# Kernel optimization log

Hardware: AMD Instinct MI355X
Metric: run time of the kernel (lower is better)

Reference implementation:

```python
import jax, jax.numpy as jnp
import numpy as np

B = 4096
MAXN = 25  # maxnfpoc, also MaxPool1d kernel size


def _w(k, fan_in, fan_out):
    return jax.random.normal(k, (fan_in, fan_out), jnp.float32) * (1.0 / np.sqrt(fan_in))


def setup_inputs() -> dict:
    key = jax.random.key(0)
    ks = jax.random.split(key, 8)
    fpoc = jax.random.normal(ks[0], (B, MAXN, 2), jnp.float32)
    nfpc = jax.random.randint(ks[1], (B,), 3, MAXN + 1, jnp.int32)
    return {
        "fpoc": fpoc,
        "cw1": _w(ks[2], 2, 64),    "cb1": jnp.zeros((64,), jnp.float32),
        "cw2": _w(ks[3], 64, 128),  "cb2": jnp.zeros((128,), jnp.float32),
        "lw1": _w(ks[4], 256, 512), "lb1": jnp.zeros((512,), jnp.float32),
        "lw2": _w(ks[5], 512, 1024),"lb2": jnp.zeros((1024,), jnp.float32),
        "fw":  _w(ks[6], 1024, 511),"fb":  jnp.zeros((511,), jnp.float32),
        "nfpc": nfpc,
    }


def reference(fpoc, cw1, cb1, cw2, cb2, lw1, lb1, lw2, lb2, fw, fb, nfpc):
    act = jax.nn.relu
    # corner MLP: act on all but last layer
    h = act(fpoc @ cw1 + cb1)
    h = h @ cw2 + cb2                               # [B, MAXN, 128]
    # vectorized ragged line pairing: (pt_i, pt_{(i+1) % nfpc}), zeros beyond nfpc
    idx = jnp.arange(MAXN)
    valid = idx[None, :] < nfpc[:, None]            # [B, MAXN]
    nxt = (idx[None, :] + 1) % nfpc[:, None]        # [B, MAXN]
    h_next = jnp.take_along_axis(h, nxt[:, :, None], axis=1)
    pair = jnp.where(valid[:, :, None], jnp.concatenate([h, h_next], axis=-1), 0.0)  # [B, MAXN, 256]
    # line MLP
    l = act(pair @ lw1 + lb1)
    l = l @ lw2 + lb2                               # [B, MAXN, 1024]
    # pad invalid slots with line 0's feature, then maxpool over all MAXN slots
    lp = jnp.where(valid[:, :, None], l, l[:, 0:1, :])
    pooled = jnp.max(lp, axis=1)                    # [B, 1024]
    # fp MLP: single linear (loop body empty for len==1), then unsqueeze
    out = pooled @ fw + fb                          # [B, 511]
    return out[:, None, :]                          # [B, 1, 511]
```

## Files before the change

### kernel.cpp

```cpp
#include <hip/hip_runtime.h>

typedef __attribute__((ext_vector_type(8))) short bf16x8;
typedef __attribute__((ext_vector_type(4))) float f32x4;
typedef __attribute__((ext_vector_type(8))) unsigned short u16x8;

#define MFMA16(a, b, c) __builtin_amdgcn_mfma_f32_16x16x32_bf16((a), (b), (c), 0, 0, 0)

static __device__ __forceinline__ unsigned short f2bf(float x) {
    union { float f; unsigned u; } v; v.f = x;
    unsigned r = v.u + 0x7fffu + ((v.u >> 16) & 1u);
    return (unsigned short)(r >> 16);
}

static __device__ __forceinline__ void gload16(const void* g, void* l) {
    __builtin_amdgcn_global_load_lds(
        (const __attribute__((address_space(1))) unsigned int*)g,
        (__attribute__((address_space(3))) unsigned int*)l, 16, 0, 0);
}

static __device__ __forceinline__ bool tile_assign(int bid, int apm, int npc_log2,
                                                   int& pr, int& pc) {
    const int k = bid & 7, j = bid >> 3;
    const int T = apm << npc_log2;
    const int lo = (T * k) >> 3, hi = (T * (k + 1)) >> 3;
    const int tix = lo + j;
    if (tix >= hi) return false;
    pc = tix & ((1 << npc_log2) - 1);
    pr = tix >> npc_log2;
    return true;
}

#define WS_POOLED   0u
#define WS_LW1T     8388608u
#define WS_LW2T     8650752u
#define WS_FWT      9699328u
#define WS_SCAN     10747904u
#define WS_HEADER   10764544u
#define WS_RMB      10764800u
#define WS_RMNEXT   11174400u
#define WS_HC       11584000u
#define WS_SCRATCH  37798400u
#define WS_HID      71352832u

__global__ void convert_scan_kernel(
    const float* __restrict__ lw1, const float* __restrict__ lw2, const float* __restrict__ fw,
    short* __restrict__ lw1t, short* __restrict__ lw2t, short* __restrict__ fwt,
    const int* __restrict__ nfpc, int* __restrict__ scanv, int* __restrict__ header)
{
    const int bid = blockIdx.x;
    const int t = threadIdx.x;
    if (bid == 288) {
        __shared__ int s[256];
        int loc[16]; int sum = 0;
        #pragma unroll
        for (int i = 0; i < 16; ++i) { loc[i] = sum; sum += nfpc[t * 16 + i]; }
        s[t] = sum;
        __syncthreads();
        for (int d = 1; d < 256; d <<= 1) {
            int v = (t >= d) ? s[t - d] : 0;
            __syncthreads();
            s[t] += v;
            __syncthreads();
        }
        int excl = (t == 0) ? 0 : s[t - 1];
        #pragma unroll
        for (int i = 0; i < 16; ++i) scanv[t * 16 + i] = excl + loc[i];
        if (t == 255) {
            int M = s[255];
            scanv[4096] = M;
            header[0] = M;
            header[1] = (M + 127) & ~127;
        }
        return;
    }

    const float* src; short* dst;
    int srcN, nmax, dstK, n0, k0;
    if (bid < 32) {
        int tn = bid >> 2, tk = bid & 3;
        src = lw1; srcN = 512; nmax = 512; dst = lw1t; dstK = 256;
        n0 = tn * 64; k0 = tk * 64;
    } else if (bid < 160) {
        int u = bid - 32; int tn = u >> 3, tk = u & 7;
        src = lw2; srcN = 1024; nmax = 1024; dst = lw2t; dstK = 512;
        n0 = tn * 64; k0 = tk * 64;
    } else {
        int u = bid - 160; int tn = u >> 4, tk = u & 15;
        src = fw; srcN = 511; nmax = 511; dst = fwt; dstK = 1024;
        n0 = tn * 64; k0 = tk * 64;
    }

    __shared__ float lds[64 * 65];
    for (int e = t; e < 4096; e += 256) {
        int r = e >> 6, c = e & 63;
        int n = n0 + c;
        lds[r * 65 + c] = (n < nmax) ? src[(size_t)(k0 + r) * srcN + n] : 0.0f;
    }
    __syncthreads();
    for (int e = t; e < 1024; e += 256) {
        int rn = e >> 4, c4 = (e & 15) * 4;
        ushort4 o;
        o.x = f2bf(lds[(c4 + 0) * 65 + rn]);
        o.y = f2bf(lds[(c4 + 1) * 65 + rn]);
        o.z = f2bf(lds[(c4 + 2) * 65 + rn]);
        o.w = f2bf(lds[(c4 + 3) * 65 + rn]);
        *(ushort4*)&dst[(size_t)(n0 + rn) * dstK + k0 + c4] = o;
    }
}

__global__ void rowmap_kernel(const int* __restrict__ scanv, const int* __restrict__ header,
                              int* __restrict__ rm_b, int* __restrict__ rm_next,
                              unsigned short* __restrict__ h_c)
{
    int r = blockIdx.x * 256 + threadIdx.x;
    if (r >= 102400) return;
    const int Mc = header[0];
    if (r >= Mc) {
        rm_b[r] = -1; rm_next[r] = r;
        if (r < header[1]) {
            ushort4 z = {0, 0, 0, 0};
            #pragma unroll
            for (int j = 0; j < 128; j += 4)
                *(ushort4*)&h_c[(size_t)r * 128 + j] = z;
        }
        return;
    }
    int lo = 0, hi = 4096;
    while (hi - lo > 1) { int mid = (lo + hi) >> 1; if (scanv[mid] <= r) lo = mid; else hi = mid; }
    int b = lo, ii = r - scanv[b], n = scanv[b + 1] - scanv[b];
    rm_b[r] = b;
    rm_next[r] = (ii + 1 == n) ? scanv[b] : r + 1;
}

#define CB 4
__global__ __launch_bounds__(256, 2) void corner_kernel(
    const float* __restrict__ fpoc,
    const float* __restrict__ cw1, const float* __restrict__ cb1,
    const float* __restrict__ cw2, const float* __restrict__ cb2,
    const int* __restrict__ scanv,
    unsigned short* __restrict__ h_c)
{
    __shared__ float s_h1[CB * 25 * 64];
    __shared__ float s_cw2[64 * 128];
    __shared__ float s_x[CB * 25 * 2];
    __shared__ int s_off[CB], s_nn[CB];
    const int b0 = blockIdx.x * CB;
    const int t = threadIdx.x;

    for (int e = t; e < 64 * 128; e += 256) s_cw2[e] = cw2[e];
    for (int e = t; e < CB * 50; e += 256) s_x[e] = fpoc[b0 * 50 + e];
    if (t < CB) { int o = scanv[b0 + t]; s_off[t] = o; s_nn[t] = scanv[b0 + t + 1] - o; }
    __syncthreads();

    for (int e = t; e < CB * 25 * 64; e += 256) {
        int i = e >> 6, j = e & 63;
        float v = s_x[i * 2] * cw1[j] + s_x[i * 2 + 1] * cw1[64 + j] + cb1[j];
        s_h1[e] = fmaxf(v, 0.f);
    }
    __syncthreads();

    for (int e = t; e < CB * 25 * 32; e += 256) {
        int i = e >> 5, j4 = (e & 31) * 4;
        int g = i / 25, ii = i % 25;
        if (ii < s_nn[g]) {
            float4 a = *(const float4*)(cb2 + j4);
            const float* h1r = &s_h1[i * 64];
            #pragma unroll
            for (int k = 0; k < 64; ++k) {
                float hv = h1r[k];
                float4 wv = *(const float4*)(s_cw2 + k * 128 + j4);
                a.x += hv * wv.x; a.y += hv * wv.y; a.z += hv * wv.z; a.w += hv * wv.w;
            }
            ushort4 o;
            o.x = f2bf(a.x); o.y = f2bf(a.y); o.z = f2bf(a.z); o.w = f2bf(a.w);
            *(ushort4*)&h_c[(size_t)(s_off[g] + ii) * 128 + j4] = o;
        }
    }
}

__global__ __launch_bounds__(256, 4) void gemm1_kernel(
    const unsigned short* __restrict__ h_c,
    const short* __restrict__ lw1t,
    const float* __restrict__ lb1,
    const int* __restrict__ rm_next,
    const int* __restrict__ header,
    unsigned short* __restrict__ hid,
    int row0, int pm)
{
    __shared__ __align__(16) char smem[33280];
    __shared__ int s_next[128];

    const int Mcp = header[1];
    int rem = Mcp - row0;
    int apm = (rem <= 0) ? 0 : min(pm, (rem + 127) >> 7);
    int pr, pc;
    if (!tile_assign(blockIdx.x, apm, 2, pr, pc)) return;
    const int Rl = pr * 128;
    const int R = row0 + Rl;

    const int t = threadIdx.x;
    const int w = t >> 6, l = t & 63, q = l >> 4, ln = l & 15;
    const int wr = w >> 1, wc = w & 1;
    char* ldsA = smem;
    char* ldsB = smem + 16384;

    if (t < 128) s_next[t] = rm_next[R + t];
    __syncthreads();

    f32x4 acc[4][4];
    #pragma unroll
    for (int m = 0; m < 4; ++m)
        #pragma unroll
        for (int n = 0; n < 4; ++n) acc[m][n] = 0;

    #pragma unroll
    for (int kt = 0; kt < 4; ++kt) {
        const int k0 = kt * 64;
        #pragma unroll
        for (int i = 0; i < 4; ++i) {
            int o = i * 4096 + t * 16;
            int row = o >> 7, colb = o & 127;
            int colb2 = colb ^ ((row & 7) << 4);
            int k = k0 + (colb2 >> 1);
            int srow, kk2;
            if (k < 128) { srow = R + row; kk2 = k; }
            else { srow = s_next[row]; kk2 = k - 128; }
            gload16(h_c + (size_t)srow * 128 + kk2, ldsA + o);
        }
        #pragma unroll
        for (int i = 0; i < 4; ++i) {
            int o = i * 4096 + t * 16;
            int row = o >> 7, colb = o & 127;
            int colb2 = colb ^ ((row & 7) << 4);
            gload16(lw1t + (size_t)(pc * 128 + row) * 256 + k0 + (colb2 >> 1), ldsB + o);
        }
        asm volatile("s_waitcnt vmcnt(0)");
        __syncthreads();
        #pragma unroll
        for (int kk = 0; kk < 2; ++kk) {
            bf16x8 af[4], bf[4];
            #pragma unroll
            for (int m = 0; m < 4; ++m) {
                int row = wr * 64 + m * 16 + ln;
                int off = (row * 128 + kk * 64 + q * 16) ^ ((row & 7) << 4);
                af[m] = *(const bf16x8*)(ldsA + off);
            }
            #pragma unroll
            for (int n = 0; n < 4; ++n) {
                int row = wc * 64 + n * 16 + ln;
                int off = (row * 128 + kk * 64 + q * 16) ^ ((row & 7) << 4);
                bf[n] = *(const bf16x8*)(ldsB + off);
            }
            #pragma unroll
            for (int m = 0; m < 4; ++m)
                #pragma unroll
                for (int n = 0; n < 4; ++n)
                    acc[m][n] = MFMA16(af[m], bf[n], acc[m][n]);
        }
        __syncthreads();
    }

    float* s_f32 = (float*)smem;
    const int erow = t >> 2;
    const int ecl = (t & 3) * 8;
    #pragma unroll 1
    for (int h = 0; h < 2; ++h) {
        if (wr == h) {
            #pragma unroll
            for (int n = 0; n < 4; ++n) {
                int col = wc * 64 + n * 16 + ln;
                float bias = lb1[pc * 128 + col];
                #pragma unroll
                for (int m = 0; m < 4; ++m)
                    #pragma unroll
                    for (int r = 0; r < 4; ++r)
                        s_f32[(m * 16 + q * 4 + r) * 130 + col] =
                            fmaxf(acc[m][n][r] + bias, 0.f);
            }
        }
        __syncthreads();
        {
            const size_t gr = (size_t)(Rl + h * 64 + erow) * 512 + pc * 128;
            #pragma unroll
            for (int j = 0; j < 4; ++j) {
                int c0 = ecl + j * 32;
                float4 a = *(const float4*)&s_f32[erow * 130 + c0];
                float4 b = *(const float4*)&s_f32[erow * 130 + c0 + 4];
                u16x8 o;
                o[0] = f2bf(a.x); o[1] = f2bf(a.y); o[2] = f2bf(a.z); o[3] = f2bf(a.w);
                o[4] = f2bf(b.x); o[5] = f2bf(b.y); o[6] = f2bf(b.z); o[7] = f2bf(b.w);
                *(u16x8*)&hid[gr + c0] = o;
            }
        }
        __syncthreads();
    }
}

__global__ __launch_bounds__(256, 4) void gemm2_kernel(
    const unsigned short* __restrict__ hid,
    const short* __restrict__ lw2t,
    const int* __restrict__ rm_b,
    const int* __restrict__ scanv,
    const int* __restrict__ header,
    float* __restrict__ scratch,
    int row0, int pm)
{
    __shared__ __align__(16) char smem[33280];
    __shared__ int s_batch[128];

    const int Mcp = header[1];
    int rem = Mcp - row0;
    int apm = (rem <= 0) ? 0 : min(pm, (rem + 127) >> 7);
    int pr, pc;
    if (!tile_assign(blockIdx.x, apm, 3, pr, pc)) return;
    const int Rl = pr * 128;
    const int R = row0 + Rl;

    const int t = threadIdx.x;
    const int w = t >> 6, l = t & 63, q = l >> 4, ln = l & 15;
    const int wr = w >> 1, wc = w & 1;
    char* ldsA = smem;
    char* ldsB = smem + 16384;

    if (t < 128) s_batch[t] = rm_b[R + t];
    __syncthreads();

    f32x4 acc[4][4];
    #pragma unroll
    for (int m = 0; m < 4; ++m)
        #pragma unroll
        for (int n = 0; n < 4; ++n) acc[m][n] = 0;

    for (int kt = 0; kt < 8; ++kt) {
        const int k0 = kt * 64;
        #pragma unroll
        for (int i = 0; i < 4; ++i) {
            int o = i * 4096 + t * 16;
            int row = o >> 7, colb = o & 127;
            int colb2 = colb ^ ((row & 7) << 4);
            gload16(hid + (size_t)(Rl + row) * 512 + k0 + (colb2 >> 1), ldsA + o);
        }
        #pragma unroll
        for (int i = 0; i < 4; ++i) {
            int o = i * 4096 + t * 16;
            int row = o >> 7, colb = o & 127;
            int colb2 = colb ^ ((row & 7) << 4);
            gload16(lw2t + (size_t)(pc * 128 + row) * 512 + k0 + (colb2 >> 1), ldsB + o);
        }
        asm volatile("s_waitcnt vmcnt(0)");
        __syncthreads();
        #pragma unroll
        for (int kk = 0; kk < 2; ++kk) {
            bf16x8 af[4], bf[4];
            #pragma unroll
            for (int m = 0; m < 4; ++m) {
                int row = wr * 64 + m * 16 + ln;
                int off = (row * 128 + kk * 64 + q * 16) ^ ((row & 7) << 4);
                af[m] = *(const bf16x8*)(ldsA + off);
            }
            #pragma unroll
            for (int n = 0; n < 4; ++n) {
                int row = wc * 64 + n * 16 + ln;
                int off = (row * 128 + kk * 64 + q * 16) ^ ((row & 7) << 4);
                bf[n] = *(const bf16x8*)(ldsB + off);
            }
            #pragma unroll
            for (int m = 0; m < 4; ++m)
                #pragma unroll
                for (int n = 0; n < 4; ++n)
                    acc[m][n] = MFMA16(af[m], bf[n], acc[m][n]);
        }
        __syncthreads();
    }

    float* s_f32 = (float*)smem;
    const int ecol = t & 127, esub = t >> 7;
    #pragma unroll 1
    for (int h = 0; h < 2; ++h) {
        if (wr == h) {
            #pragma unroll
            for (int m = 0; m < 4; ++m)
                #pragma unroll
                for (int n = 0; n < 4; ++n)
                    #pragma unroll
                    for (int r = 0; r < 4; ++r)
                        s_f32[(m * 16 + q * 4 + r) * 130 + wc * 64 + n * 16 + ln] = acc[m][n][r];
        }
        __syncthreads();
        {
            const int ub = R + h * 64 + esub * 32;
            const int rb = h * 64 + esub * 32;
            const int lb = esub * 32;
            int curb = s_batch[rb];
            float curmax = s_f32[lb * 130 + ecol];
            #pragma unroll 8
            for (int row = 1; row < 32; ++row) {
                int b = s_batch[rb + row];
                float v = s_f32[(lb + row) * 130 + ecol];
                if (b == curb) {
                    curmax = fmaxf(curmax, v);
                } else {
                    if (curb >= 0) {
                        int slot = (scanv[curb] < ub) ? 1 : 0;
                        scratch[((size_t)curb * 2 + slot) * 1024 + pc * 128 + ecol] = curmax;
                    }
                    curb = b;
                    curmax = v;
                }
            }
            if (curb >= 0) {
                int slot = (scanv[curb] < ub) ? 1 : 0;
                scratch[((size_t)curb * 2 + slot) * 1024 + pc * 128 + ecol] = curmax;
            }
        }
        __syncthreads();
    }
}

__global__ void merge_kernel(const float* __restrict__ scratch, const int* __restrict__ scanv,
                             const float* __restrict__ lb2, unsigned short* __restrict__ pooled_b)
{
    const int b = blockIdx.x;
    const int col4 = threadIdx.x * 4;
    const int o0 = scanv[b], o1 = scanv[b + 1];
    const bool spans = (o0 >> 5) != ((o1 - 1) >> 5);
    float4 v = *(const float4*)&scratch[((size_t)b * 2) * 1024 + col4];
    if (spans) {
        float4 u = *(const float4*)&scratch[((size_t)b * 2 + 1) * 1024 + col4];
        v.x = fmaxf(v.x, u.x); v.y = fmaxf(v.y, u.y);
        v.z = fmaxf(v.z, u.z); v.w = fmaxf(v.w, u.w);
    }
    float4 bb = *(const float4*)(lb2 + col4);
    ushort4 o;
    o.x = f2bf(v.x + bb.x); o.y = f2bf(v.y + bb.y);
    o.z = f2bf(v.z + bb.z); o.w = f2bf(v.w + bb.w);
    *(ushort4*)&pooled_b[(size_t)b * 1024 + col4] = o;
}

__global__ __launch_bounds__(512, 2) void final_kernel(
    const unsigned short* __restrict__ pooled_b,
    const short* __restrict__ fwt,
    const float* __restrict__ fb,
    float* __restrict__ out)
{
    const int tid = threadIdx.x;
    const int w = tid >> 6, l = tid & 63, q = l >> 4, ln = l & 15;
    const int rb = blockIdx.x * 128 + w * 16;
    const int nb0 = blockIdx.y * 64;

    f32x4 acc[4];
    #pragma unroll
    for (int j = 0; j < 4; ++j) acc[j] = 0;

    const short* pb = (const short*)pooled_b;
    #pragma unroll 4
    for (int ks = 0; ks < 32; ++ks) {
        bf16x8 a = *(const bf16x8*)(pb + (rb + ln) * 1024 + ks * 32 + q * 8);
        #pragma unroll
        for (int j = 0; j < 4; ++j) {
            bf16x8 bf = *(const bf16x8*)(fwt + (nb0 + j * 16 + ln) * 1024 + ks * 32 + q * 8);
            acc[j] = MFMA16(a, bf, acc[j]);
        }
    }
    #pragma unroll
    for (int j = 0; j < 4; ++j) {
        int col = nb0 + j * 16 + ln;
        if (col < 511) {
            float bias = fb[col];
            #pragma unroll
            for (int r = 0; r < 4; ++r) {
                int row = rb + q * 4 + r;
                out[row * 511 + col] = acc[j][r] + bias;
            }
        }
    }
}

extern "C" void kernel_launch(void* const* d_in, const int* in_sizes, int n_in,
                              void* d_out, int out_size, void* d_ws, size_t ws_size,
                              hipStream_t stream)
{
    const float* fpoc = (const float*)d_in[0];
    const float* cw1  = (const float*)d_in[1];
    const float* cb1  = (const float*)d_in[2];
    const float* cw2  = (const float*)d_in[3];
    const float* cb2  = (const float*)d_in[4];
    const float* lw1  = (const float*)d_in[5];
    const float* lb1  = (const float*)d_in[6];
    const float* lw2  = (const float*)d_in[7];
    const float* lb2  = (const float*)d_in[8];
    const float* fw   = (const float*)d_in[9];
    const float* fb   = (const float*)d_in[10];
    const int*  nfpc  = (const int*)d_in[11];

    char* ws = (char*)d_ws;
    unsigned short* pooled_b = (unsigned short*)(ws + WS_POOLED);
    short* lw1t   = (short*)(ws + WS_LW1T);
    short* lw2t   = (short*)(ws + WS_LW2T);
    short* fwt    = (short*)(ws + WS_FWT);
    int*   scanv  = (int*)(ws + WS_SCAN);
    int*   header = (int*)(ws + WS_HEADER);
    int*   rm_b   = (int*)(ws + WS_RMB);
    int*   rm_next= (int*)(ws + WS_RMNEXT);
    unsigned short* h_c = (unsigned short*)(ws + WS_HC);
    float* scratch = (float*)(ws + WS_SCRATCH);
    unsigned short* hid = (unsigned short*)(ws + WS_HID);

    size_t avail = (ws_size > WS_HID) ? ws_size - WS_HID : 0;
    int n_chunks = 1;
    while (n_chunks < 16 && (size_t)(104857600u / n_chunks) > avail) n_chunks <<= 1;
    const int crows = 102400 / n_chunks;
    const int pm = crows / 128;

    hipLaunchKernelGGL(convert_scan_kernel, dim3(289), dim3(256), 0, stream,
                       lw1, lw2, fw, lw1t, lw2t, fwt, nfpc, scanv, header);
    hipLaunchKernelGGL(rowmap_kernel, dim3(400), dim3(256), 0, stream,
                       scanv, header, rm_b, rm_next, h_c);
    hipLaunchKernelGGL(corner_kernel, dim3(1024), dim3(256), 0, stream,
                       fpoc, cw1, cb1, cw2, cb2, scanv, h_c);
    const int g1 = ((pm * 4 + 7) / 8) * 8;
    const int g2 = pm * 8;
    for (int c = 0; c < n_chunks; ++c) {
        int row0 = c * crows;
        hipLaunchKernelGGL(gemm1_kernel, dim3(g1), dim3(256), 0, stream,
                           h_c, lw1t, lb1, rm_next, header, hid, row0, pm);
        hipLaunchKernelGGL(gemm2_kernel, dim3(g2), dim3(256), 0, stream,
                           hid, lw2t, rm_b, scanv, header, scratch, row0, pm);
    }
    hipLaunchKernelGGL(merge_kernel, dim3(4096), dim3(256), 0, stream,
                       scratch, scanv, lb2, pooled_b);
    hipLaunchKernelGGL(final_kernel, dim3(32, 8), dim3(512), 0, stream,
                       pooled_b, fwt, fb, (float*)d_out);
}
```

Before: 212.0 us.

## Fuse weight conversion, scan, rowmap and corner MLP into one prep kernel

Merges the convert/scan, rowmap and corner kernels into a single launch. Blocks are split by ID into weight transpose, global scan, rowmap (each block recomputes the full scan in LDS) and corner MLP (each block computes its own prefix offset by reduction, and reads cw2 straight from global memory instead of staging it in LDS). This removes two launches and their serialization, at the cost of redundant scan work per block. Separately, final_kernel now computes 128 columns per block instead of 64, halving the grid and reusing each A-fragment load across more MFMAs.

```diff
diff --git a/kernel.cpp b/kernel.cpp
--- a/kernel.cpp
+++ b/kernel.cpp
@@ -42,15 +42,59 @@
 #define WS_SCRATCH  37798400u
 #define WS_HID      71352832u
 
-__global__ void convert_scan_kernel(
+#define CB 4
+
+__global__ __launch_bounds__(256) void prep_kernel(
     const float* __restrict__ lw1, const float* __restrict__ lw2, const float* __restrict__ fw,
     short* __restrict__ lw1t, short* __restrict__ lw2t, short* __restrict__ fwt,
-    const int* __restrict__ nfpc, int* __restrict__ scanv, int* __restrict__ header)
+    const int* __restrict__ nfpc, int* __restrict__ scanv, int* __restrict__ header,
+    const float* __restrict__ fpoc,
+    const float* __restrict__ cw1, const float* __restrict__ cb1,
+    const float* __restrict__ cw2, const float* __restrict__ cb2,
+    int* __restrict__ rm_b, int* __restrict__ rm_next,
+    unsigned short* __restrict__ h_c)
 {
+    __shared__ __align__(16) char pmem[27776];
     const int bid = blockIdx.x;
     const int t = threadIdx.x;
+
+    if (bid < 288) {
+        const float* src; short* dst;
+        int srcN, nmax, dstK, n0, k0;
+        if (bid < 32) {
+            int tn = bid >> 2, tk = bid & 3;
+            src = lw1; srcN = 512; nmax = 512; dst = lw1t; dstK = 256;
+            n0 = tn * 64; k0 = tk * 64;
+        } else if (bid < 160) {
+            int u = bid - 32; int tn = u >> 3, tk = u & 7;
+            src = lw2; srcN = 1024; nmax = 1024; dst = lw2t; dstK = 512;
+            n0 = tn * 64; k0 = tk * 64;
+        } else {
+            int u = bid - 160; int tn = u >> 4, tk = u & 15;
+            src = fw; srcN = 511; nmax = 511; dst = fwt; dstK = 1024;
+            n0 = tn * 64; k0 = tk * 64;
+        }
+        float* lds = (float*)pmem;
+        for (int e = t; e < 4096; e += 256) {
+            int r = e >> 6, c = e & 63;
+            int n = n0 + c;
+            lds[r * 65 + c] = (n < nmax) ? src[(size_t)(k0 + r) * srcN + n] : 0.0f;
+        }
+        __syncthreads();
+        for (int e = t; e < 1024; e += 256) {
+            int rn = e >> 4, c4 = (e & 15) * 4;
+            ushort4 o;
+            o.x = f2bf(lds[(c4 + 0) * 65 + rn]);
+            o.y = f2bf(lds[(c4 + 1) * 65 + rn]);
+            o.z = f2bf(lds[(c4 + 2) * 65 + rn]);
+            o.w = f2bf(lds[(c4 + 3) * 65 + rn]);
+            *(ushort4*)&dst[(size_t)(n0 + rn) * dstK + k0 + c4] = o;
+        }
+        return;
+    }
+
     if (bid == 288) {
-        __shared__ int s[256];
+        int* s = (int*)pmem;
         int loc[16]; int sum = 0;
         #pragma unroll
         for (int i = 0; i < 16; ++i) { loc[i] = sum; sum += nfpc[t * 16 + i]; }
@@ -74,106 +118,106 @@
         return;
     }
 
-    const float* src; short* dst;
-    int srcN, nmax, dstK, n0, k0;
-    if (bid < 32) {
-        int tn = bid >> 2, tk = bid & 3;
-        src = lw1; srcN = 512; nmax = 512; dst = lw1t; dstK = 256;
-        n0 = tn * 64; k0 = tk * 64;
-    } else if (bid < 160) {
-        int u = bid - 32; int tn = u >> 3, tk = u & 7;
-        src = lw2; srcN = 1024; nmax = 1024; dst = lw2t; dstK = 512;
-        n0 = tn * 64; k0 = tk * 64;
-    } else {
-        int u = bid - 160; int tn = u >> 4, tk = u & 15;
-        src = fw; srcN = 511; nmax = 511; dst = fwt; dstK = 1024;
-        n0 = tn * 64; k0 = tk * 64;
-    }
-
-    __shared__ float lds[64 * 65];
-    for (int e = t; e < 4096; e += 256) {
-        int r = e >> 6, c = e & 63;
-        int n = n0 + c;
-        lds[r * 65 + c] = (n < nmax) ? src[(size_t)(k0 + r) * srcN + n] : 0.0f;
-    }
-    __syncthreads();
-    for (int e = t; e < 1024; e += 256) {
-        int rn = e >> 4, c4 = (e & 15) * 4;
-        ushort4 o;
-        o.x = f2bf(lds[(c4 + 0) * 65 + rn]);
-        o.y = f2bf(lds[(c4 + 1) * 65 + rn]);
-        o.z = f2bf(lds[(c4 + 2) * 65 + rn]);
-        o.w = f2bf(lds[(c4 + 3) * 65 + rn]);
-        *(ushort4*)&dst[(size_t)(n0 + rn) * dstK + k0 + c4] = o;
-    }
-}
-
-__global__ void rowmap_kernel(const int* __restrict__ scanv, const int* __restrict__ header,
-                              int* __restrict__ rm_b, int* __restrict__ rm_next,
-                              unsigned short* __restrict__ h_c)
-{
-    int r = blockIdx.x * 256 + threadIdx.x;
-    if (r >= 102400) return;
-    const int Mc = header[0];
-    if (r >= Mc) {
-        rm_b[r] = -1; rm_next[r] = r;
-        if (r < header[1]) {
-            ushort4 z = {0, 0, 0, 0};
-            #pragma unroll
-            for (int j = 0; j < 128; j += 4)
-                *(ushort4*)&h_c[(size_t)r * 128 + j] = z;
-        }
+    if (bid < 689) {
+        int* s_scan = (int*)pmem;
+        int* s_red  = (int*)(pmem + 16400);
+        int loc[16]; int sum = 0;
+        #pragma unroll
+        for (int i = 0; i < 16; ++i) { loc[i] = sum; sum += nfpc[t * 16 + i]; }
+        s_red[t] = sum;
+        __syncthreads();
+        for (int d = 1; d < 256; d <<= 1) {
+            int v = (t >= d) ? s_red[t - d] : 0;
+            __syncthreads();
+            s_red[t] += v;
+            __syncthreads();
+        }
+        int excl = (t == 0) ? 0 : s_red[t - 1];
+        #pragma unroll
+        for (int i = 0; i < 16; ++i) s_scan[t * 16 + i] = excl + loc[i];
+        if (t == 255) s_scan[4096] = s_red[255];
+        __syncthreads();
+
+        const int Mc = s_scan[4096];
+        const int Mcp = (Mc + 127) & ~127;
+        int r = (bid - 289) * 256 + t;
+        if (r >= 102400) return;
+        if (r >= Mc) {
+            rm_b[r] = -1; rm_next[r] = r;
+            if (r < Mcp) {
+                ushort4 z = {0, 0, 0, 0};
+                #pragma unroll
+                for (int j = 0; j < 128; j += 4)
+                    *(ushort4*)&h_c[(size_t)r * 128 + j] = z;
+            }
+            return;
+        }
+        int lo = 0, hi = 4096;
+        while (hi - lo > 1) { int mid = (lo + hi) >> 1; if (s_scan[mid] <= r) lo = mid; else hi = mid; }
+        int b = lo, ii = r - s_scan[b], n = s_scan[b + 1] - s_scan[b];
+        rm_b[r] = b;
+        rm_next[r] = (ii + 1 == n) ? s_scan[b] : r + 1;
         return;
     }
-    int lo = 0, hi = 4096;
-    while (hi - lo > 1) { int mid = (lo + hi) >> 1; if (scanv[mid] <= r) lo = mid; else hi = mid; }
-    int b = lo, ii = r - scanv[b], n = scanv[b + 1] - scanv[b];
-    rm_b[r] = b;
-    rm_next[r] = (ii + 1 == n) ? scanv[b] : r + 1;
-}
-
-#define CB 4
-__global__ __launch_bounds__(256, 2) void corner_kernel(
-    const float* __restrict__ fpoc,
-    const float* __restrict__ cw1, const float* __restrict__ cb1,
-    const float* __restrict__ cw2, const float* __restrict__ cb2,
-    const int* __restrict__ scanv,
-    unsigned short* __restrict__ h_c)
-{
-    __shared__ float s_h1[CB * 25 * 64];
-    __shared__ float s_cw2[64 * 128];
-    __shared__ float s_x[CB * 25 * 2];
-    __shared__ int s_off[CB], s_nn[CB];
-    const int b0 = blockIdx.x * CB;
-    const int t = threadIdx.x;
-
-    for (int e = t; e < 64 * 128; e += 256) s_cw2[e] = cw2[e];
-    for (int e = t; e < CB * 50; e += 256) s_x[e] = fpoc[b0 * 50 + e];
-    if (t < CB) { int o = scanv[b0 + t]; s_off[t] = o; s_nn[t] = scanv[b0 + t + 1] - o; }
-    __syncthreads();
-
-    for (int e = t; e < CB * 25 * 64; e += 256) {
-        int i = e >> 6, j = e & 63;
-        float v = s_x[i * 2] * cw1[j] + s_x[i * 2 + 1] * cw1[64 + j] + cb1[j];
-        s_h1[e] = fmaxf(v, 0.f);
-    }
-    __syncthreads();
-
-    for (int e = t; e < CB * 25 * 32; e += 256) {
-        int i = e >> 5, j4 = (e & 31) * 4;
-        int g = i / 25, ii = i % 25;
-        if (ii < s_nn[g]) {
-            float4 a = *(const float4*)(cb2 + j4);
-            const float* h1r = &s_h1[i * 64];
-            #pragma unroll
-            for (int k = 0; k < 64; ++k) {
-                float hv = h1r[k];
-                float4 wv = *(const float4*)(s_cw2 + k * 128 + j4);
-                a.x += hv * wv.x; a.y += hv * wv.y; a.z += hv * wv.z; a.w += hv * wv.w;
-            }
-            ushort4 o;
-            o.x = f2bf(a.x); o.y = f2bf(a.y); o.z = f2bf(a.z); o.w = f2bf(a.w);
-            *(ushort4*)&h_c[(size_t)(s_off[g] + ii) * 128 + j4] = o;
+
+    {
+        const int cb = bid - 689;
+        const int b0 = cb * CB;
+        float* s_h1 = (float*)pmem;
+        float* s_x  = (float*)(pmem + 25600);
+        int* s_red  = (int*)(pmem + 26400);
+        int* s_off  = (int*)(pmem + 27424);
+        int* s_nn   = (int*)(pmem + 27424 + CB * 4);
+
+        int partial = 0;
+        const int c0 = t * 16;
+        #pragma unroll
+        for (int i = 0; i < 16; ++i) {
+            int idx = c0 + i;
+            partial += (idx < b0) ? nfpc[idx] : 0;
+        }
+        s_red[t] = partial;
+        for (int e = t; e < CB * 50; e += 256) s_x[e] = fpoc[b0 * 50 + e];
+        __syncthreads();
+        for (int d = 128; d > 0; d >>= 1) {
+            if (t < d) s_red[t] += s_red[t + d];
+            __syncthreads();
+        }
+        if (t == 0) {
+            int o = s_red[0];
+            #pragma unroll
+            for (int g = 0; g < CB; ++g) {
+                s_off[g] = o;
+                int nn = nfpc[b0 + g];
+                s_nn[g] = nn;
+                o += nn;
+            }
+        }
+        __syncthreads();
+
+        for (int e = t; e < CB * 25 * 64; e += 256) {
+            int i = e >> 6, j = e & 63;
+            float v = s_x[i * 2] * cw1[j] + s_x[i * 2 + 1] * cw1[64 + j] + cb1[j];
+            s_h1[e] = fmaxf(v, 0.f);
+        }
+        __syncthreads();
+
+        for (int e = t; e < CB * 25 * 32; e += 256) {
+            int i = e >> 5, j4 = (e & 31) * 4;
+            int g = i / 25, ii = i % 25;
+            if (ii < s_nn[g]) {
+                float4 a = *(const float4*)(cb2 + j4);
+                const float* h1r = &s_h1[i * 64];
+                #pragma unroll
+                for (int k = 0; k < 64; ++k) {
+                    float hv = h1r[k];
+                    float4 wv = *(const float4*)(cw2 + k * 128 + j4);
+                    a.x += hv * wv.x; a.y += hv * wv.y; a.z += hv * wv.z; a.w += hv * wv.w;
+                }
+                ushort4 o;
+                o.x = f2bf(a.x); o.y = f2bf(a.y); o.z = f2bf(a.z); o.w = f2bf(a.w);
+                *(ushort4*)&h_c[(size_t)(s_off[g] + ii) * 128 + j4] = o;
+            }
         }
     }
 }
@@ -446,24 +490,24 @@
     const int tid = threadIdx.x;
     const int w = tid >> 6, l = tid & 63, q = l >> 4, ln = l & 15;
     const int rb = blockIdx.x * 128 + w * 16;
-    const int nb0 = blockIdx.y * 64;
-
-    f32x4 acc[4];
+    const int nb0 = blockIdx.y * 128;
+
+    f32x4 acc[8];
     #pragma unroll
-    for (int j = 0; j < 4; ++j) acc[j] = 0;
+    for (int j = 0; j < 8; ++j) acc[j] = 0;
 
     const short* pb = (const short*)pooled_b;
-    #pragma unroll 4
+    #pragma unroll 2
     for (int ks = 0; ks < 32; ++ks) {
         bf16x8 a = *(const bf16x8*)(pb + (rb + ln) * 1024 + ks * 32 + q * 8);
         #pragma unroll
-        for (int j = 0; j < 4; ++j) {
+        for (int j = 0; j < 8; ++j) {
             bf16x8 bf = *(const bf16x8*)(fwt + (nb0 + j * 16 + ln) * 1024 + ks * 32 + q * 8);
             acc[j] = MFMA16(a, bf, acc[j]);
         }
     }
     #pragma unroll
-    for (int j = 0; j < 4; ++j) {
+    for (int j = 0; j < 8; ++j) {
         int col = nb0 + j * 16 + ln;
         if (col < 511) {
             float bias = fb[col];
@@ -512,12 +556,9 @@
     const int crows = 102400 / n_chunks;
     const int pm = crows / 128;
 
-    hipLaunchKernelGGL(convert_scan_kernel, dim3(289), dim3(256), 0, stream,
-                       lw1, lw2, fw, lw1t, lw2t, fwt, nfpc, scanv, header);
-    hipLaunchKernelGGL(rowmap_kernel, dim3(400), dim3(256), 0, stream,
-                       scanv, header, rm_b, rm_next, h_c);
-    hipLaunchKernelGGL(corner_kernel, dim3(1024), dim3(256), 0, stream,
-                       fpoc, cw1, cb1, cw2, cb2, scanv, h_c);
+    hipLaunchKernelGGL(prep_kernel, dim3(1713), dim3(256), 0, stream,
+                       lw1, lw2, fw, lw1t, lw2t, fwt, nfpc, scanv, header,
+                       fpoc, cw1, cb1, cw2, cb2, rm_b, rm_next, h_c);
     const int g1 = ((pm * 4 + 7) / 8) * 8;
     const int g2 = pm * 8;
     for (int c = 0; c < n_chunks; ++c) {
@@ -529,6 +570,6 @@
     }
     hipLaunchKernelGGL(merge_kernel, dim3(4096), dim3(256), 0, stream,
                        scratch, scanv, lb2, pooled_b);
-    hipLaunchKernelGGL(final_kernel, dim3(32, 8), dim3(512), 0, stream,
+    hipLaunchKernelGGL(final_kernel, dim3(32, 4), dim3(512), 0, stream,
                        pooled_b, fwt, fb, (float*)d_out);
 }
```

Result: slower. 263.4 us (+24.2%).
